# Kernel optimization log

Hardware: AMD Instinct MI355X
Metric: run time of the kernel (lower is better)

Reference implementation:

```python
import jax, jax.numpy as jnp
import numpy as np
from jax import lax

B, H, L, DK = 8, 8, 1024, 64
BN_EPS = 1e-5


def _conv_bn_sm(x, w, b, g, beta, pad):
    # x: [B, H, L] (N=batch, C=h heads as channels, spatial=L)
    y = lax.conv_general_dilated(x, w, (1,), [(pad, pad)], dimension_numbers=("NCH", "OIH", "NCH"))
    y = y + b[None, :, None]
    # BatchNorm1d in training mode: batch stats over (N, L) per channel, biased var
    mu = jnp.mean(y, axis=(0, 2), keepdims=True)
    var = jnp.var(y, axis=(0, 2), keepdims=True)
    y = (y - mu) * (g[None, :, None] / jnp.sqrt(var + BN_EPS)) + beta[None, :, None]
    return jax.nn.softmax(y, axis=-1)


def setup_inputs() -> dict:
    key = jax.random.key(0)
    ks = jax.random.split(key, 20)
    n = lambda i, shape, s=1.0: jax.random.normal(ks[i], shape, dtype=jnp.float32) * s
    inp = {
        "Q": n(0, (B, H, L, DK)),
        "K": n(1, (B, H, L, DK)),
        "V": n(2, (B, H, L, DK)),
        "attn_mask": jnp.ones((1,), dtype=bool),
        # proj_q / proj_k: Linear(d_k, 1, bias=False) weight [1, d_k] -> stored as [d_k]
        "wq": n(3, (DK,), 0.1), "wk": n(4, (DK,), 0.1),
        # proj_back_q / proj_back_k: Linear(1, d_k, bias=False) weight [d_k, 1] -> [d_k]
        "wbq": n(5, (DK,), 0.1), "wbk": n(6, (DK,), 0.1),
        # Conv1d(h, h, f) weights [out=h, in=h, f] + bias [h]
        "cq3_w": n(7, (H, H, 3), 0.2), "cq3_b": n(8, (H,), 0.05),
        "cq9_w": n(9, (H, H, 9), 0.1), "cq9_b": n(10, (H,), 0.05),
        "ck3_w": n(11, (H, H, 3), 0.2), "ck3_b": n(12, (H,), 0.05),
        "ck9_w": n(13, (H, H, 9), 0.1), "ck9_b": n(14, (H,), 0.05),
        # BatchNorm1d affine params
        "bnq3_g": jnp.ones((H,), jnp.float32), "bnq3_b": jnp.zeros((H,), jnp.float32),
        "bnq9_g": jnp.ones((H,), jnp.float32), "bnq9_b": jnp.zeros((H,), jnp.float32),
        "bnk3_g": jnp.ones((H,), jnp.float32), "bnk3_b": jnp.zeros((H,), jnp.float32),
        "bnk9_g": jnp.ones((H,), jnp.float32), "bnk9_b": jnp.zeros((H,), jnp.float32),
    }
    return inp


def reference(Q, K, V, attn_mask, wq, wk, wbq, wbk,
              cq3_w, cq3_b, cq9_w, cq9_b, ck3_w, ck3_b, ck9_w, ck9_b,
              bnq3_g, bnq3_b, bnq9_g, bnq9_b, bnk3_g, bnk3_b, bnk9_g, bnk9_b):
    b, h, l, d_k = Q.shape
    l_k = K.shape[2]
    # proj to scalar per position, reshape to [b, h, l]
    Qp = jnp.einsum("bhld,d->bhl", Q, wq)
    Kp = jnp.einsum("bhld,d->bhl", K, wk)
    # multi-scale conv + BN(train) + softmax branches
    q0 = _conv_bn_sm(Qp, cq3_w, cq3_b, bnq3_g, bnq3_b, 1)
    q1 = _conv_bn_sm(Qp, cq9_w, cq9_b, bnq9_g, bnq9_b, 4)
    k0 = _conv_bn_sm(Kp, ck3_w, ck3_b, bnk3_g, bnk3_b, 1)
    k1 = _conv_bn_sm(Kp, ck9_w, ck9_b, bnk9_g, bnk9_b, 4)
    # faithful to torch: cat along dim 0 then C-order reshape to [b,h,l,2], max over last
    Qm = jnp.max(jnp.concatenate([q0, q1], axis=0).reshape(b, h, l, 2), axis=-1)
    Km = jnp.max(jnp.concatenate([k0, k1], axis=0).reshape(b, h, l_k, 2), axis=-1)
    # proj back 1 -> d_k (no bias): outer with weight vector
    Qn = Qm[..., None] * wbq  # [b,h,l,d_k]
    Kn = Km[..., None] * wbk  # [b,h,l_k,d_k]
    scores = jnp.einsum("bhqd,bhkd->bhqk", Qn, Kn) / jnp.sqrt(jnp.float32(d_k))
    attn = jax.nn.softmax(scores, axis=-1)
    context = jnp.einsum("bhqk,bhkd->bhqd", attn, V)
    return (context, attn)
```

## Files before the change

kernel.cpp:

```cpp
#include <hip/hip_runtime.h>

constexpr int SL = 1024;
constexpr int NBH = 64;

constexpr int QP_OFF = 0;
constexpr int KP_OFF = 65536;
constexpr int Y_OFF  = 131072;
constexpr int QM_OFF = 655360;
constexpr int KM_OFF = 720896;
constexpr int ST_OFF = 786432;
constexpr int C_OFF  = 786496;
constexpr int VT_OFF = 786560;

typedef __attribute__((ext_vector_type(8))) short short8;
typedef __attribute__((ext_vector_type(4))) float f32x4;

__device__ inline unsigned short f2bf(float x) {
    unsigned int u = __float_as_uint(x);
    unsigned int r = (u + 0x7fff + ((u >> 16) & 1)) >> 16;
    return (unsigned short)r;
}

__global__ __launch_bounds__(256) void k_projpack(
    const float* __restrict__ Q, const float* __restrict__ K,
    const float* __restrict__ V,
    const float* __restrict__ wq, const float* __restrict__ wk,
    const float* __restrict__ wbq, const float* __restrict__ wbk,
    float* __restrict__ ws)
{
    int b = blockIdx.x;
    int tid = threadIdx.x;
    if (b < 8192) {
        bool isQ = b < 4096;
        const float* src = isQ ? Q : K;
        const float* w   = isQ ? wq : wk;
        int row = (b - (isQ ? 0 : 4096)) * 16 + (tid >> 4);
        int l16 = tid & 15;
        float4 x  = ((const float4*)(src + row * 64))[l16];
        float4 w4 = ((const float4*)w)[l16];
        float v = x.x * w4.x + x.y * w4.y + x.z * w4.z + x.w * w4.w;
        #pragma unroll
        for (int m = 8; m; m >>= 1) v += __shfl_xor(v, m);
        if (l16 == 0) ws[(isQ ? QP_OFF : KP_OFF) + row] = v;
    } else if (b < 10240) {
        int t = (b - 8192) * 256 + tid;
        int lane = t & 63;
        int s    = (t >> 6) & 7;
        int dsub = (t >> 9) & 3;
        int chunk= (t >> 11) & 3;
        int bh   = t >> 13;
        const float* vb = V + bh * (SL * 64);
        int k0 = chunk * 256 + s * 32 + (lane >> 4) * 8;
        int d  = dsub * 16 + (lane & 15);
        unsigned short o[8];
        #pragma unroll
        for (int j = 0; j < 8; j++) o[j] = f2bf(vb[(k0 + j) * 64 + d]);
        unsigned short* vt = (unsigned short*)(ws + VT_OFF);
        *(short8*)(vt + (size_t)t * 8) = *(short8*)o;
    } else {
        if (tid < 64) {
            ws[ST_OFF + tid] = 0.f;
            float v = wbq[tid] * wbk[tid];
            #pragma unroll
            for (int m = 32; m; m >>= 1) v += __shfl_xor(v, m);
            if (tid == 0) ws[C_OFF] = v * 0.125f;
        }
    }
}

__global__ __launch_bounds__(256) void k_conv(
    float* __restrict__ ws,
    const float* __restrict__ w0, const float* __restrict__ b0,
    const float* __restrict__ w1, const float* __restrict__ b1,
    const float* __restrict__ w2, const float* __restrict__ b2,
    const float* __restrict__ w3, const float* __restrict__ b3)
{
    int branch = blockIdx.x >> 6;
    int n = (blockIdx.x >> 3) & 7;
    int seg = blockIdx.x & 7;
    int t0 = seg * 128;
    const float* wp = branch == 0 ? w0 : branch == 1 ? w1 : branch == 2 ? w2 : w3;
    const float* bp = branch == 0 ? b0 : branch == 1 ? b1 : branch == 2 ? b2 : b3;
    const int F = (branch & 1) ? 9 : 3;
    const int PAD = F >> 1;
    const float* x = ws + ((branch < 2) ? QP_OFF : KP_OFF) + n * 8 * SL;

    __shared__ float xl[8][136];
    __shared__ float wl[8 * 8 * 9];
    __shared__ float bl[8];
    int tid = threadIdx.x;
    for (int i = tid; i < 8 * 8 * F; i += 256) wl[i] = wp[i];
    if (tid < 8) bl[tid] = bp[tid];
    for (int i = tid; i < 8 * 136; i += 256) {
        int ci = i / 136; int tt = i - ci * 136;
        int ta = t0 + tt - 4;
        xl[ci][tt] = (ta >= 0 && ta < SL) ? x[ci * SL + ta] : 0.f;
    }
    __syncthreads();
    int c = tid >> 5, u = tid & 31;
    float s1 = 0.f, s2 = 0.f;
    float* yout = ws + Y_OFF + branch * (NBH * SL) + (n * 8 + c) * SL + t0;
    #pragma unroll
    for (int q = 0; q < 4; q++) {
        int tl = q * 32 + u;
        float acc = bl[c];
        for (int ci = 0; ci < 8; ci++) {
            const float* xr = &xl[ci][tl + 4 - PAD];
            const float* wr = &wl[(c * 8 + ci) * F];
            for (int f = 0; f < F; f++) acc += wr[f] * xr[f];
        }
        yout[tl] = acc;
        s1 += acc; s2 += acc * acc;
    }
    #pragma unroll
    for (int m = 16; m; m >>= 1) {
        s1 += __shfl_xor(s1, m);
        s2 += __shfl_xor(s2, m);
    }
    if (u == 0) {
        atomicAdd(&ws[ST_OFF + (branch * 8 + c) * 2],     s1);
        atomicAdd(&ws[ST_OFF + (branch * 8 + c) * 2 + 1], s2);
    }
}

__global__ __launch_bounds__(256) void k_bnmix(
    float* __restrict__ ws,
    const float* __restrict__ g0, const float* __restrict__ be0,
    const float* __restrict__ g1, const float* __restrict__ be1,
    const float* __restrict__ g2, const float* __restrict__ be2,
    const float* __restrict__ g3, const float* __restrict__ be3)
{
    int blk = blockIdx.x;
    int which = blk >> 6;
    int i = (blk >> 3) & 7, j = blk & 7;
    int n = 2 * i + (j >= 4 ? 1 : 0);
    int br = which * 2 + (n >= 8 ? 1 : 0);
    int row = n & 7;
    int tid = threadIdx.x;
    int half = tid >> 7;
    int u = tid & 127;
    int c = 2 * (j & 3) + half;
    const float* gp = br == 0 ? g0 : br == 1 ? g1 : br == 2 ? g2 : g3;
    const float* bp = br == 0 ? be0 : br == 1 ? be1 : br == 2 ? be2 : be3;
    float s1 = ws[ST_OFF + (br * 8 + c) * 2];
    float s2 = ws[ST_OFF + (br * 8 + c) * 2 + 1];
    float mu  = s1 * (1.f / 8192.f);
    float var = s2 * (1.f / 8192.f) - mu * mu;
    float sc = gp[c] * rsqrtf(var + 1e-5f);
    float sh = bp[c] - mu * sc;
    const float* y = ws + Y_OFF + br * (NBH * SL) + (row * 8 + c) * SL;
    float4 ya = ((const float4*)y)[u * 2];
    float4 yb = ((const float4*)y)[u * 2 + 1];
    float z[8] = { ya.x * sc + sh, ya.y * sc + sh, ya.z * sc + sh, ya.w * sc + sh,
                   yb.x * sc + sh, yb.y * sc + sh, yb.z * sc + sh, yb.w * sc + sh };
    float mx = z[0];
    #pragma unroll
    for (int q = 1; q < 8; q++) mx = fmaxf(mx, z[q]);
    __shared__ float r1[4], r2[4];
    #pragma unroll
    for (int m = 32; m; m >>= 1) mx = fmaxf(mx, __shfl_xor(mx, m));
    if ((tid & 63) == 0) r1[tid >> 6] = mx;
    __syncthreads();
    mx = half ? fmaxf(r1[2], r1[3]) : fmaxf(r1[0], r1[1]);
    float e[8];
    float s = 0.f;
    #pragma unroll
    for (int q = 0; q < 8; q++) { e[q] = __expf(z[q] - mx); s += e[q]; }
    #pragma unroll
    for (int m = 32; m; m >>= 1) s += __shfl_xor(s, m);
    if ((tid & 63) == 0) r2[tid >> 6] = s;
    __syncthreads();
    s = half ? (r2[2] + r2[3]) : (r2[0] + r2[1]);
    float inv = 1.f / s;
    float4 o = make_float4(fmaxf(e[0], e[1]) * inv, fmaxf(e[2], e[3]) * inv,
                           fmaxf(e[4], e[5]) * inv, fmaxf(e[6], e[7]) * inv);
    float* outp = ws + (which ? KM_OFF : QM_OFF) + i * 8192 + j * 1024 + half * 512;
    ((float4*)outp)[u] = o;
}

__global__ __launch_bounds__(256, 4) void k_attn(
    float* __restrict__ out, const float* __restrict__ ws)
{
    int p = blockIdx.x;
    int xcd = p & 7, idx = p >> 3;
    int bh = xcd + 8 * (idx >> 6);
    int qt = idx & 63;
    int tid = threadIdx.x;

    __shared__ __align__(16) float kml[1024];
    __shared__ float aql[16], mql[16];
    __shared__ float rmx[4], rmn[4];
    __shared__ float wsum[4][16];
    __shared__ float accred[4][16][64];

    const float* km = ws + KM_OFF + bh * SL;
    const float* qm = ws + QM_OFF + bh * SL + qt * 16;
    float c = ws[C_OFF];

    float lmax = -1e30f, lmin = 1e30f;
    #pragma unroll
    for (int i = 0; i < 4; i++) {
        float v = km[tid + 256 * i];
        kml[tid + 256 * i] = v;
        lmax = fmaxf(lmax, v); lmin = fminf(lmin, v);
    }
    #pragma unroll
    for (int m = 32; m; m >>= 1) {
        lmax = fmaxf(lmax, __shfl_xor(lmax, m));
        lmin = fminf(lmin, __shfl_xor(lmin, m));
    }
    if ((tid & 63) == 0) { rmx[tid >> 6] = lmax; rmn[tid >> 6] = lmin; }
    __syncthreads();
    if (tid < 16) {
        float kmax = fmaxf(fmaxf(rmx[0], rmx[1]), fmaxf(rmx[2], rmx[3]));
        float kmin = fminf(fminf(rmn[0], rmn[1]), fminf(rmn[2], rmn[3]));
        float a = c * qm[tid];
        aql[tid] = a;
        mql[tid] = (a > 0.f) ? a * kmax : a * kmin;
    }
    __syncthreads();

    int w = tid >> 6, lane = tid & 63;
    int m16 = lane & 15, kg = lane >> 4;
    float a = aql[m16], mm = mql[m16];

    float e[64];
    float rowsum = 0.f;
    #pragma unroll
    for (int s = 0; s < 8; s++) {
        const float4* kp = (const float4*)(kml + w * 256 + s * 32 + kg * 8);
        float4 ka = kp[0], kb = kp[1];
        e[s * 8 + 0] = __expf(a * ka.x - mm);
        e[s * 8 + 1] = __expf(a * ka.y - mm);
        e[s * 8 + 2] = __expf(a * ka.z - mm);
        e[s * 8 + 3] = __expf(a * ka.w - mm);
        e[s * 8 + 4] = __expf(a * kb.x - mm);
        e[s * 8 + 5] = __expf(a * kb.y - mm);
        e[s * 8 + 6] = __expf(a * kb.z - mm);
        e[s * 8 + 7] = __expf(a * kb.w - mm);
        #pragma unroll
        for (int j = 0; j < 8; j++) rowsum += e[s * 8 + j];
    }
    rowsum += __shfl_xor(rowsum, 16);
    rowsum += __shfl_xor(rowsum, 32);
    if (lane < 16) wsum[w][lane] = rowsum;
    __syncthreads();
    float rr = 1.f / (wsum[0][m16] + wsum[1][m16] + wsum[2][m16] + wsum[3][m16]);

    float* attn_row = out + 4194304 + ((size_t)(bh * SL + qt * 16 + m16)) * SL;
    const short8* vt8 = (const short8*)((const unsigned short*)(ws + VT_OFF))
                        + (size_t)bh * 8192 + w * 2048;

    f32x4 acc0 = {0,0,0,0}, acc1 = {0,0,0,0}, acc2 = {0,0,0,0}, acc3 = {0,0,0,0};

    #pragma unroll
    for (int s = 0; s < 8; s++) {
        int k0 = w * 256 + s * 32 + kg * 8;
        float es[8];
        #pragma unroll
        for (int j = 0; j < 8; j++) es[j] = e[s * 8 + j] * rr;
        *(float4*)(attn_row + k0)     = make_float4(es[0], es[1], es[2], es[3]);
        *(float4*)(attn_row + k0 + 4) = make_float4(es[4], es[5], es[6], es[7]);
        unsigned short af[8];
        #pragma unroll
        for (int j = 0; j < 8; j++) af[j] = f2bf(es[j]);
        short8 av = *(short8*)af;
        const short8* bbase = vt8 + s * 64 + lane;
        short8 b0 = bbase[0 * 512];
        short8 b1 = bbase[1 * 512];
        short8 b2 = bbase[2 * 512];
        short8 b3 = bbase[3 * 512];
        acc0 = __builtin_amdgcn_mfma_f32_16x16x32_bf16(av, b0, acc0, 0, 0, 0);
        acc1 = __builtin_amdgcn_mfma_f32_16x16x32_bf16(av, b1, acc1, 0, 0, 0);
        acc2 = __builtin_amdgcn_mfma_f32_16x16x32_bf16(av, b2, acc2, 0, 0, 0);
        acc3 = __builtin_amdgcn_mfma_f32_16x16x32_bf16(av, b3, acc3, 0, 0, 0);
    }

    #pragma unroll
    for (int reg = 0; reg < 4; reg++) {
        int r = kg * 4 + reg;
        accred[w][r][ 0 + m16] = acc0[reg];
        accred[w][r][16 + m16] = acc1[reg];
        accred[w][r][32 + m16] = acc2[reg];
        accred[w][r][48 + m16] = acc3[reg];
    }
    __syncthreads();
    {
        int r  = tid >> 4;
        int d0 = (tid & 15) * 4;
        float4 s0 = *(const float4*)&accred[0][r][d0];
        float4 s1 = *(const float4*)&accred[1][r][d0];
        float4 s2 = *(const float4*)&accred[2][r][d0];
        float4 s3 = *(const float4*)&accred[3][r][d0];
        float4 o = make_float4(s0.x + s1.x + s2.x + s3.x,
                               s0.y + s1.y + s2.y + s3.y,
                               s0.z + s1.z + s2.z + s3.z,
                               s0.w + s1.w + s2.w + s3.w);
        float* ctx = out + ((size_t)(bh * SL + qt * 16 + r)) * 64 + d0;
        *(float4*)ctx = o;
    }
}

extern "C" void kernel_launch(void* const* d_in, const int* in_sizes, int n_in,
                              void* d_out, int out_size, void* d_ws, size_t ws_size,
                              hipStream_t stream)
{
    const float* Q      = (const float*)d_in[0];
    const float* K      = (const float*)d_in[1];
    const float* V      = (const float*)d_in[2];
    const float* wq     = (const float*)d_in[4];
    const float* wk     = (const float*)d_in[5];
    const float* wbq    = (const float*)d_in[6];
    const float* wbk    = (const float*)d_in[7];
    const float* cq3_w  = (const float*)d_in[8];
    const float* cq3_b  = (const float*)d_in[9];
    const float* cq9_w  = (const float*)d_in[10];
    const float* cq9_b  = (const float*)d_in[11];
    const float* ck3_w  = (const float*)d_in[12];
    const float* ck3_b  = (const float*)d_in[13];
    const float* ck9_w  = (const float*)d_in[14];
    const float* ck9_b  = (const float*)d_in[15];
    const float* bnq3_g = (const float*)d_in[16];
    const float* bnq3_b = (const float*)d_in[17];
    const float* bnq9_g = (const float*)d_in[18];
    const float* bnq9_b = (const float*)d_in[19];
    const float* bnk3_g = (const float*)d_in[20];
    const float* bnk3_b = (const float*)d_in[21];
    const float* bnk9_g = (const float*)d_in[22];
    const float* bnk9_b = (const float*)d_in[23];
    float* out = (float*)d_out;
    float* ws  = (float*)d_ws;

    k_projpack<<<10241, 256, 0, stream>>>(Q, K, V, wq, wk, wbq, wbk, ws);
    k_conv<<<256, 256, 0, stream>>>(ws, cq3_w, cq3_b, cq9_w, cq9_b,
                                    ck3_w, ck3_b, ck9_w, ck9_b);
    k_bnmix<<<128, 256, 0, stream>>>(ws, bnq3_g, bnq3_b, bnq9_g, bnq9_b,
                                     bnk3_g, bnk3_b, bnk9_g, bnk9_b);
    k_attn<<<4096, 256, 0, stream>>>(out, ws);
}
```

Before: 394.4 us.

## Recompute conv in bnmix instead of storing intermediate conv output

The conv kernel now only accumulates BatchNorm statistics and no longer writes its full output to workspace. The bnmix kernel reloads the projected rows into shared memory and recomputes the convolution for its two channels before normalization and softmax. This removes a round trip of the intermediate tensor through global memory at the cost of doing the convolution twice and using more shared memory in bnmix. Separately, the attention kernel computes the per-row scale and max offset directly in each thread, dropping one barrier, and its launch-bounds occupancy hint goes from 4 to 3.

```diff
diff --git a/kernel.cpp b/kernel.cpp
--- a/kernel.cpp
+++ b/kernel.cpp
@@ -5,7 +5,6 @@
 
 constexpr int QP_OFF = 0;
 constexpr int KP_OFF = 65536;
-constexpr int Y_OFF  = 131072;
 constexpr int QM_OFF = 655360;
 constexpr int KM_OFF = 720896;
 constexpr int ST_OFF = 786432;
@@ -68,7 +67,7 @@
     }
 }
 
-__global__ __launch_bounds__(256) void k_conv(
+__global__ __launch_bounds__(256) void k_stats(
     float* __restrict__ ws,
     const float* __restrict__ w0, const float* __restrict__ b0,
     const float* __restrict__ w1, const float* __restrict__ b1,
@@ -99,7 +98,6 @@
     __syncthreads();
     int c = tid >> 5, u = tid & 31;
     float s1 = 0.f, s2 = 0.f;
-    float* yout = ws + Y_OFF + branch * (NBH * SL) + (n * 8 + c) * SL + t0;
     #pragma unroll
     for (int q = 0; q < 4; q++) {
         int tl = q * 32 + u;
@@ -109,7 +107,6 @@
             const float* wr = &wl[(c * 8 + ci) * F];
             for (int f = 0; f < F; f++) acc += wr[f] * xr[f];
         }
-        yout[tl] = acc;
         s1 += acc; s2 += acc * acc;
     }
     #pragma unroll
@@ -125,6 +122,10 @@
 
 __global__ __launch_bounds__(256) void k_bnmix(
     float* __restrict__ ws,
+    const float* __restrict__ w0, const float* __restrict__ b0,
+    const float* __restrict__ w1, const float* __restrict__ b1,
+    const float* __restrict__ w2, const float* __restrict__ b2,
+    const float* __restrict__ w3, const float* __restrict__ b3,
     const float* __restrict__ g0, const float* __restrict__ be0,
     const float* __restrict__ g1, const float* __restrict__ be1,
     const float* __restrict__ g2, const float* __restrict__ be2,
@@ -139,24 +140,61 @@
     int tid = threadIdx.x;
     int half = tid >> 7;
     int u = tid & 127;
-    int c = 2 * (j & 3) + half;
+    int c0 = 2 * (j & 3);
+    int c = c0 + half;
+    const int F = (br & 1) ? 9 : 3;
+    const int PAD = F >> 1;
+    const float* cw = br == 0 ? w0 : br == 1 ? w1 : br == 2 ? w2 : w3;
+    const float* cb = br == 0 ? b0 : br == 1 ? b1 : br == 2 ? b2 : b3;
     const float* gp = br == 0 ? g0 : br == 1 ? g1 : br == 2 ? g2 : g3;
     const float* bp = br == 0 ? be0 : br == 1 ? be1 : br == 2 ? be2 : be3;
+
+    __shared__ float xl[8][1036];
+    __shared__ float wl2[2][72];
+    __shared__ float bl2[2];
+    __shared__ float r1[4], r2[4];
+
+    if (tid < 2 * 8 * F) {
+        int cc = tid / (8 * F);
+        int k  = tid - cc * (8 * F);
+        wl2[cc][k] = cw[(c0 + cc) * 8 * F + k];
+    }
+    if (tid < 2) bl2[tid] = cb[c0 + tid];
+    const float* x = ws + ((br < 2) ? QP_OFF : KP_OFF) + row * 8 * SL;
+    #pragma unroll
+    for (int ci = 0; ci < 8; ci++)
+        for (int t = tid; t < 1032; t += 256) {
+            int ta = t - 4;
+            xl[ci][t] = (ta >= 0 && ta < SL) ? x[ci * SL + ta] : 0.f;
+        }
+    __syncthreads();
+
+    float z[8];
+    int p0 = u * 8;
+    const float* wr0 = wl2[half];
+    #pragma unroll
+    for (int q = 0; q < 8; q++) {
+        float acc = bl2[half];
+        for (int ci = 0; ci < 8; ci++) {
+            const float* xr = &xl[ci][p0 + q + 4 - PAD];
+            const float* wr = wr0 + ci * F;
+            for (int f = 0; f < F; f++) acc += wr[f] * xr[f];
+        }
+        z[q] = acc;
+    }
+
     float s1 = ws[ST_OFF + (br * 8 + c) * 2];
     float s2 = ws[ST_OFF + (br * 8 + c) * 2 + 1];
     float mu  = s1 * (1.f / 8192.f);
     float var = s2 * (1.f / 8192.f) - mu * mu;
     float sc = gp[c] * rsqrtf(var + 1e-5f);
     float sh = bp[c] - mu * sc;
-    const float* y = ws + Y_OFF + br * (NBH * SL) + (row * 8 + c) * SL;
-    float4 ya = ((const float4*)y)[u * 2];
-    float4 yb = ((const float4*)y)[u * 2 + 1];
-    float z[8] = { ya.x * sc + sh, ya.y * sc + sh, ya.z * sc + sh, ya.w * sc + sh,
-                   yb.x * sc + sh, yb.y * sc + sh, yb.z * sc + sh, yb.w * sc + sh };
+    #pragma unroll
+    for (int q = 0; q < 8; q++) z[q] = z[q] * sc + sh;
+
     float mx = z[0];
     #pragma unroll
     for (int q = 1; q < 8; q++) mx = fmaxf(mx, z[q]);
-    __shared__ float r1[4], r2[4];
     #pragma unroll
     for (int m = 32; m; m >>= 1) mx = fmaxf(mx, __shfl_xor(mx, m));
     if ((tid & 63) == 0) r1[tid >> 6] = mx;
@@ -178,7 +216,7 @@
     ((float4*)outp)[u] = o;
 }
 
-__global__ __launch_bounds__(256, 4) void k_attn(
+__global__ __launch_bounds__(256, 3) void k_attn(
     float* __restrict__ out, const float* __restrict__ ws)
 {
     int p = blockIdx.x;
@@ -188,7 +226,6 @@
     int tid = threadIdx.x;
 
     __shared__ __align__(16) float kml[1024];
-    __shared__ float aql[16], mql[16];
     __shared__ float rmx[4], rmn[4];
     __shared__ float wsum[4][16];
     __shared__ float accred[4][16][64];
@@ -211,18 +248,13 @@
     }
     if ((tid & 63) == 0) { rmx[tid >> 6] = lmax; rmn[tid >> 6] = lmin; }
     __syncthreads();
-    if (tid < 16) {
-        float kmax = fmaxf(fmaxf(rmx[0], rmx[1]), fmaxf(rmx[2], rmx[3]));
-        float kmin = fminf(fminf(rmn[0], rmn[1]), fminf(rmn[2], rmn[3]));
-        float a = c * qm[tid];
-        aql[tid] = a;
-        mql[tid] = (a > 0.f) ? a * kmax : a * kmin;
-    }
-    __syncthreads();
 
     int w = tid >> 6, lane = tid & 63;
     int m16 = lane & 15, kg = lane >> 4;
-    float a = aql[m16], mm = mql[m16];
+    float kmax = fmaxf(fmaxf(rmx[0], rmx[1]), fmaxf(rmx[2], rmx[3]));
+    float kmin = fminf(fminf(rmn[0], rmn[1]), fminf(rmn[2], rmn[3]));
+    float a = c * qm[m16];
+    float mm = (a > 0.f) ? a * kmax : a * kmin;
 
     float e[64];
     float rowsum = 0.f;
@@ -332,9 +364,11 @@
     float* ws  = (float*)d_ws;
 
     k_projpack<<<10241, 256, 0, stream>>>(Q, K, V, wq, wk, wbq, wbk, ws);
-    k_conv<<<256, 256, 0, stream>>>(ws, cq3_w, cq3_b, cq9_w, cq9_b,
-                                    ck3_w, ck3_b, ck9_w, ck9_b);
-    k_bnmix<<<128, 256, 0, stream>>>(ws, bnq3_g, bnq3_b, bnq9_g, bnq9_b,
+    k_stats<<<256, 256, 0, stream>>>(ws, cq3_w, cq3_b, cq9_w, cq9_b,
+                                     ck3_w, ck3_b, ck9_w, ck9_b);
+    k_bnmix<<<128, 256, 0, stream>>>(ws, cq3_w, cq3_b, cq9_w, cq9_b,
+                                     ck3_w, ck3_b, ck9_w, ck9_b,
+                                     bnq3_g, bnq3_b, bnq9_g, bnq9_b,
                                      bnk3_g, bnk3_b, bnk9_g, bnk9_b);
     k_attn<<<4096, 256, 0, stream>>>(out, ws);
 }
```

Result: slower. 419.9 us (+6.5%).
